# Kernel optimization log

Measured on AMD Instinct MI355X. Metric: run time of the kernel, lower is better.

Reference implementation:

```python
import jax, jax.numpy as jnp
import numpy as np

N_LINKS = 10000
N_PATHS = 50000
PLEN = 5                 # fixed path length -> max_len
E = N_PATHS * PLEN       # number of (link, path) edge entries
D = 32                   # link_state_dim == path_state_dim
H = 32
RU = 256                 # readout_units
T_ITERS = 8              # message-passing iterations t


def setup_inputs() -> dict:
    key = jax.random.key(0)
    ks = jax.random.split(key, 20)
    s = 0.1
    inp = {}
    inp["traffic"] = jax.random.uniform(ks[0], (N_PATHS,), dtype=jnp.float32)
    inp["packets"] = jax.random.uniform(ks[1], (N_PATHS,), dtype=jnp.float32)
    inp["time_dist_params"] = jax.random.normal(ks[2], (N_PATHS, 12), dtype=jnp.float32)
    inp["capacity"] = jax.random.uniform(ks[3], (N_LINKS,), dtype=jnp.float32)
    # edge lists: each path has exactly PLEN links
    inp["link_to_path"] = jax.random.randint(ks[4], (E,), 0, N_LINKS, dtype=jnp.int32)
    inp["path_ids"] = jnp.repeat(jnp.arange(N_PATHS, dtype=jnp.int32), PLEN)
    inp["sequence_path"] = jnp.tile(jnp.arange(PLEN, dtype=jnp.int32), N_PATHS)
    inp["path_to_link"] = jax.random.randint(ks[5], (E,), 0, N_PATHS, dtype=jnp.int32)
    inp["sequence_links"] = jax.random.randint(ks[6], (E,), 0, N_LINKS, dtype=jnp.int32)
    inp["n_links"] = N_LINKS
    inp["n_paths"] = N_PATHS
    # path-update GRU (input D -> hidden H), torch layout [3H, in]
    inp["Wi_p"] = jax.random.normal(ks[7], (3 * H, D), dtype=jnp.float32) * s
    inp["Wh_p"] = jax.random.normal(ks[8], (3 * H, H), dtype=jnp.float32) * s
    inp["bi_p"] = jnp.zeros((3 * H,), jnp.float32)
    inp["bh_p"] = jnp.zeros((3 * H,), jnp.float32)
    # link-update GRUCell (input H -> hidden D)
    inp["Wi_l"] = jax.random.normal(ks[9], (3 * D, H), dtype=jnp.float32) * s
    inp["Wh_l"] = jax.random.normal(ks[10], (3 * D, D), dtype=jnp.float32) * s
    inp["bi_l"] = jnp.zeros((3 * D,), jnp.float32)
    inp["bh_l"] = jnp.zeros((3 * D,), jnp.float32)
    # readout MLP
    inp["W1"] = jax.random.normal(ks[11], (RU, H), dtype=jnp.float32) * s
    inp["b1"] = jnp.zeros((RU,), jnp.float32)
    inp["W2"] = jax.random.normal(ks[12], (RU, RU), dtype=jnp.float32) * s
    inp["b2"] = jnp.zeros((RU,), jnp.float32)
    inp["W3"] = jax.random.normal(ks[13], (1, RU), dtype=jnp.float32) * s
    inp["b3"] = jnp.zeros((1,), jnp.float32)
    return inp


def _gru_step(x, h, Wi, Wh, bi, bh):
    # torch GRU gate math
    gi = x @ Wi.T + bi
    gh = h @ Wh.T + bh
    ir, iz, in_ = jnp.split(gi, 3, axis=-1)
    hr, hz, hn = jnp.split(gh, 3, axis=-1)
    r = jax.nn.sigmoid(ir + hr)
    z = jax.nn.sigmoid(iz + hz)
    n = jnp.tanh(in_ + r * hn)
    return (1.0 - z) * n + z * h


def reference(traffic, packets, time_dist_params, capacity,
              link_to_path, path_ids, sequence_path, path_to_link, sequence_links,
              n_links, n_paths,
              Wi_p, Wh_p, bi_p, bh_p, Wi_l, Wh_l, bi_l, bh_l,
              W1, b1, W2, b2, W3, b3):
    max_len = PLEN  # == sequence_path.max() + 1 (static)
    # per-path valid lengths (equivalent to the torch nonzero-row count loop)
    lens = jax.ops.segment_max(sequence_path, path_ids, num_segments=n_paths) + 1
    link_state = jnp.concatenate(
        [capacity[:, None], jnp.zeros((n_links, D - 1), capacity.dtype)], axis=1)
    path_state = jnp.concatenate(
        [traffic[:, None], packets[:, None], time_dist_params,
         jnp.zeros((n_paths, D - 14), traffic.dtype)], axis=1)

    for _ in range(T_ITERS):
        link_gather = link_state[link_to_path]  # [E, D]
        link_inputs = jnp.zeros((n_paths, max_len, D), link_state.dtype)
        link_inputs = link_inputs.at[path_ids, sequence_path].set(link_gather)

        def step(h, xt_t):
            xt, t = xt_t
            h_new = _gru_step(xt, h, Wi_p, Wh_p, bi_p, bh_p)
            h = jnp.where((t < lens)[:, None], h_new, h)  # pack_padded semantics
            return h, None

        path_state, _ = jax.lax.scan(
            step, path_state,
            (jnp.swapaxes(link_inputs, 0, 1), jnp.arange(max_len)))

        path_gather = path_state[path_to_link]  # [E, H]
        path_sum = jnp.zeros((n_links, H), path_gather.dtype).at[sequence_links].add(path_gather)
        link_state = _gru_step(path_sum, link_state, Wi_l, Wh_l, bi_l, bh_l)

    r = jax.nn.relu(path_state @ W1.T + b1)
    r = jax.nn.relu(r @ W2.T + b2)
    r = r @ W3.T + b3            # [n_paths, 1]
    return r[:, 0][None, :]      # [1, n_paths]
```

## Files before the change

### kernel.cpp

```cpp
#include <hip/hip_runtime.h>

#define NP 50000
#define NL 10000
#define PLEN 5
#define NE (NP * PLEN)
#define DD 32
#define RUU 256
#define TITERS 8
#define PPB 16
#define LPB 16
#define RPB 32

__device__ __forceinline__ float sigmoidf_(float a) {
    return 1.0f / (1.0f + __expf(-a));
}
__device__ __forceinline__ float tanhf_(float a) {
    a = fminf(fmaxf(a, -15.0f), 15.0f);
    float t = __expf(2.0f * a);
    return (t - 1.0f) / (t + 1.0f);
}

__global__ __launch_bounds__(256) void k_init(
    const float* __restrict__ traffic, const float* __restrict__ packets,
    const float* __restrict__ tdp, const float* __restrict__ capacity,
    float* __restrict__ path_state, float* __restrict__ link_state,
    int* __restrict__ lens, int* __restrict__ cnt) {
    int i = blockIdx.x * 256 + threadIdx.x;
    if (i < NP) {
        float v[DD];
        v[0] = traffic[i];
        v[1] = packets[i];
#pragma unroll
        for (int k = 0; k < 12; k++) v[2 + k] = tdp[i * 12 + k];
#pragma unroll
        for (int k = 14; k < DD; k++) v[k] = 0.0f;
#pragma unroll
        for (int k = 0; k < DD; k++) path_state[i * DD + k] = v[k];
        lens[i] = 0;
    }
    if (i < NL) {
        link_state[i * DD] = capacity[i];
#pragma unroll
        for (int k = 1; k < DD; k++) link_state[i * DD + k] = 0.0f;
        cnt[i] = 0;
    }
}

__global__ __launch_bounds__(256) void k_lens(const int* __restrict__ path_ids,
                                              const int* __restrict__ seq_path,
                                              int* __restrict__ lens) {
    int e = blockIdx.x * 256 + threadIdx.x;
    if (e < NE) atomicMax(&lens[path_ids[e]], seq_path[e] + 1);
}

__global__ __launch_bounds__(256) void k_csr_count(const int* __restrict__ seq_links,
                                                   int* __restrict__ cnt) {
    int e = blockIdx.x * 256 + threadIdx.x;
    if (e < NE) atomicAdd(&cnt[seq_links[e]], 1);
}

__global__ __launch_bounds__(256) void k_csr_scan(const int* __restrict__ cnt,
                                                  int* __restrict__ offs,
                                                  int* __restrict__ cursor) {
    __shared__ int ssum[256];
    const int tid = threadIdx.x;
    const int CH = 40;
    int base = tid * CH;
    int s = 0;
    for (int i = 0; i < CH; i++) {
        int idx = base + i;
        s += (idx < NL) ? cnt[idx] : 0;
    }
    ssum[tid] = s;
    __syncthreads();
    for (int off = 1; off < 256; off <<= 1) {
        int t = (tid >= off) ? ssum[tid - off] : 0;
        __syncthreads();
        ssum[tid] += t;
        __syncthreads();
    }
    int run = ssum[tid] - s;
    for (int i = 0; i < CH; i++) {
        int idx = base + i;
        if (idx < NL) {
            offs[idx] = run;
            cursor[idx] = run;
            run += cnt[idx];
        }
    }
    if (tid == 0) offs[NL] = ssum[255];
}

__global__ __launch_bounds__(256) void k_csr_fill(const int* __restrict__ seq_links,
                                                  const int* __restrict__ path_to_link,
                                                  int* __restrict__ cursor,
                                                  int* __restrict__ csr_pids) {
    int e = blockIdx.x * 256 + threadIdx.x;
    if (e < NE) {
        int l = seq_links[e];
        int slot = atomicAdd(&cursor[l], 1);
        csr_pids[slot] = path_to_link[e];
    }
}

__global__ __launch_bounds__(256) void k_w2t(const float* __restrict__ W2,
                                             float* __restrict__ W2t) {
    int j = blockIdx.x, k = threadIdx.x;
    W2t[k * RUU + j] = W2[j * RUU + k];
}

__global__ __launch_bounds__(256, 4) void k_gru_paths(
    const float* __restrict__ link_state, float* __restrict__ path_state,
    const int* __restrict__ link_to_path, const int* __restrict__ lens,
    const float* __restrict__ Wi, const float* __restrict__ Wh,
    const float* __restrict__ bi, const float* __restrict__ bh) {
    __shared__ float gi[PPB * PLEN * 96];
    __shared__ float hbuf[4][DD];
    const int tid = threadIdx.x;
    const int wave = tid >> 6;
    const int lane = tid & 63;
    const int d = lane & 31;
    const int half = lane >> 5;
    const int pl0 = wave * 4;
    const int pbase = blockIdx.x * PPB;

    float w[3][16];
#pragma unroll
    for (int g = 0; g < 3; g++) {
        const float* wp = &Wi[(g * 32 + d) * 32 + half * 16];
#pragma unroll
        for (int c = 0; c < 4; c++) *(float4*)&w[g][c * 4] = *(const float4*)&wp[c * 4];
    }
#pragma unroll
    for (int g = 0; g < 3; g++)
#pragma unroll
        for (int k = 0; k < 16; k++) asm volatile("" : "+v"(w[g][k]));
    {
        const float b0 = bi[d], b1_ = bi[d + 32], b2_ = bi[d + 64];
        for (int j = 0; j < 4; j++) {
            const int p = pbase + pl0 + j;
#pragma unroll
            for (int st = 0; st < PLEN; st++) {
                const int li = link_to_path[p * PLEN + st];
                float xk[16];
#pragma unroll
                for (int c = 0; c < 4; c++)
                    *(float4*)&xk[c * 4] =
                        *(const float4*)&link_state[li * DD + half * 16 + c * 4];
                float s0 = 0.f, s1 = 0.f, s2 = 0.f;
#pragma unroll
                for (int k = 0; k < 16; k++) {
                    s0 = fmaf(xk[k], w[0][k], s0);
                    s1 = fmaf(xk[k], w[1][k], s1);
                    s2 = fmaf(xk[k], w[2][k], s2);
                }
                s0 += __shfl_xor(s0, 32);
                s1 += __shfl_xor(s1, 32);
                s2 += __shfl_xor(s2, 32);
                float* gp = &gi[((pl0 + j) * PLEN + st) * 96];
                gp[d]      = s0 + b0;
                gp[d + 32] = s1 + b1_;
                gp[d + 64] = s2 + b2_;
            }
        }
    }
    __syncthreads();

#pragma unroll
    for (int g = 0; g < 3; g++) {
        const float* wp = &Wh[(g * 32 + d) * 32 + half * 16];
#pragma unroll
        for (int c = 0; c < 4; c++) *(float4*)&w[g][c * 4] = *(const float4*)&wp[c * 4];
    }
#pragma unroll
    for (int g = 0; g < 3; g++)
#pragma unroll
        for (int k = 0; k < 16; k++) asm volatile("" : "+v"(w[g][k]));
    const float bh0 = bh[d], bh1 = bh[d + 32], bh2 = bh[d + 64];

    for (int j = 0; j < 4; j++) {
        const int p = pbase + pl0 + j;
        const int len = lens[p];
        float hd = path_state[p * DD + d];
        float hk[16];
#pragma unroll
        for (int c = 0; c < 4; c++)
            *(float4*)&hk[c * 4] = *(const float4*)&path_state[p * DD + half * 16 + c * 4];
#pragma unroll
        for (int st = 0; st < PLEN; st++) {
            float hr = 0.f, hz = 0.f, hn = 0.f;
#pragma unroll
            for (int k = 0; k < 16; k++) {
                hr = fmaf(hk[k], w[0][k], hr);
                hz = fmaf(hk[k], w[1][k], hz);
                hn = fmaf(hk[k], w[2][k], hn);
            }
            hr += __shfl_xor(hr, 32);
            hz += __shfl_xor(hz, 32);
            hn += __shfl_xor(hn, 32);
            const float* gp = &gi[((pl0 + j) * PLEN + st) * 96];
            float gir = gp[d], giz = gp[d + 32], gin = gp[d + 64];
            float r = sigmoidf_(gir + hr + bh0);
            float z = sigmoidf_(giz + hz + bh1);
            float n = tanhf_(gin + r * (hn + bh2));
            float hnew = (1.0f - z) * n + z * hd;
            hd = (st < len) ? hnew : hd;
            hbuf[wave][d] = hd;
#pragma unroll
            for (int c = 0; c < 4; c++)
                *(float4*)&hk[c * 4] = *(const float4*)&hbuf[wave][half * 16 + c * 4];
        }
        if (half == 0) path_state[p * DD + d] = hd;
    }
}

__global__ __launch_bounds__(256, 4) void k_links(
    const float* __restrict__ path_state, float* __restrict__ link_state,
    const int* __restrict__ offs, const int* __restrict__ csr_pids,
    const float* __restrict__ Wi, const float* __restrict__ Wh,
    const float* __restrict__ bi, const float* __restrict__ bh) {
    __shared__ float xsum[4][4][DD];
    __shared__ float gil[4][4][96];
    const int tid = threadIdx.x;
    const int wave = tid >> 6;
    const int lane = tid & 63;
    const int d = lane & 31;
    const int half = lane >> 5;
    const int lbase = blockIdx.x * LPB + wave * 4;

    for (int j = 0; j < 4; j++) {
        const int l = lbase + j;
        const int beg = offs[l], end = offs[l + 1];
        float xv = 0.f;
        int t = beg + half;
        int pid = (t < end) ? csr_pids[t] : 0;
        while (t < end) {
            int t2 = t + 2;
            int pid2 = (t2 < end) ? csr_pids[t2] : 0;
            xv += path_state[pid * DD + d];
            pid = pid2;
            t = t2;
        }
        xv += __shfl_xor(xv, 32);
        xsum[wave][j][d] = xv;
    }
    __syncthreads();

    float w[3][16];
#pragma unroll
    for (int g = 0; g < 3; g++) {
        const float* wp = &Wi[(g * 32 + d) * 32 + half * 16];
#pragma unroll
        for (int c = 0; c < 4; c++) *(float4*)&w[g][c * 4] = *(const float4*)&wp[c * 4];
    }
#pragma unroll
    for (int g = 0; g < 3; g++)
#pragma unroll
        for (int k = 0; k < 16; k++) asm volatile("" : "+v"(w[g][k]));
    {
        const float b0 = bi[d], b1_ = bi[d + 32], b2_ = bi[d + 64];
        for (int j = 0; j < 4; j++) {
            float xk[16];
#pragma unroll
            for (int c = 0; c < 4; c++)
                *(float4*)&xk[c * 4] = *(const float4*)&xsum[wave][j][half * 16 + c * 4];
            float s0 = 0.f, s1 = 0.f, s2 = 0.f;
#pragma unroll
            for (int k = 0; k < 16; k++) {
                s0 = fmaf(xk[k], w[0][k], s0);
                s1 = fmaf(xk[k], w[1][k], s1);
                s2 = fmaf(xk[k], w[2][k], s2);
            }
            s0 += __shfl_xor(s0, 32);
            s1 += __shfl_xor(s1, 32);
            s2 += __shfl_xor(s2, 32);
            gil[wave][j][d]      = s0 + b0;
            gil[wave][j][d + 32] = s1 + b1_;
            gil[wave][j][d + 64] = s2 + b2_;
        }
    }
    __syncthreads();

#pragma unroll
    for (int g = 0; g < 3; g++) {
        const float* wp = &Wh[(g * 32 + d) * 32 + half * 16];
#pragma unroll
        for (int c = 0; c < 4; c++) *(float4*)&w[g][c * 4] = *(const float4*)&wp[c * 4];
    }
#pragma unroll
    for (int g = 0; g < 3; g++)
#pragma unroll
        for (int k = 0; k < 16; k++) asm volatile("" : "+v"(w[g][k]));
    const float bh0 = bh[d], bh1 = bh[d + 32], bh2 = bh[d + 64];
    for (int j = 0; j < 4; j++) {
        const int l = lbase + j;
        float hd = link_state[l * DD + d];
        float hk[16];
#pragma unroll
        for (int c = 0; c < 4; c++)
            *(float4*)&hk[c * 4] = *(const float4*)&link_state[l * DD + half * 16 + c * 4];
        float hr = 0.f, hz = 0.f, hn = 0.f;
#pragma unroll
        for (int k = 0; k < 16; k++) {
            hr = fmaf(hk[k], w[0][k], hr);
            hz = fmaf(hk[k], w[1][k], hz);
            hn = fmaf(hk[k], w[2][k], hn);
        }
        hr += __shfl_xor(hr, 32);
        hz += __shfl_xor(hz, 32);
        hn += __shfl_xor(hn, 32);
        float gir = gil[wave][j][d], giz = gil[wave][j][d + 32], gin = gil[wave][j][d + 64];
        float r = sigmoidf_(gir + hr + bh0);
        float z = sigmoidf_(giz + hz + bh1);
        float n = tanhf_(gin + r * (hn + bh2));
        float hnew = (1.0f - z) * n + z * hd;
        if (half == 0) link_state[l * DD + d] = hnew;
    }
}

__global__ __launch_bounds__(256, 4) void k_readout(
    const float* __restrict__ path_state, float* __restrict__ out,
    const float* __restrict__ W1, const float* __restrict__ b1,
    const float* __restrict__ W2t, const float* __restrict__ b2,
    const float* __restrict__ W3, const float* __restrict__ b3) {
    __shared__ float sr1[RPB * RUU];
    const int tid = threadIdx.x;
    const int p0 = blockIdx.x * RPB;

    float w1r[DD];
#pragma unroll
    for (int c = 0; c < 8; c++)
        *(float4*)&w1r[c * 4] = *(const float4*)&W1[tid * DD + c * 4];
    float bb1 = b1[tid];

#pragma unroll 2
    for (int m = 0; m < RPB; m++) {
        int p = p0 + m;
        if (p >= NP) p = NP - 1;
        const float4* xr = (const float4*)&path_state[(size_t)p * DD];
        float acc = bb1;
#pragma unroll
        for (int c = 0; c < 8; c++) {
            float4 xv = xr[c];
            acc = fmaf(xv.x, w1r[c * 4 + 0], fmaf(xv.y, w1r[c * 4 + 1],
                  fmaf(xv.z, w1r[c * 4 + 2], fmaf(xv.w, w1r[c * 4 + 3], acc))));
        }
        sr1[m * RUU + tid] = fmaxf(acc, 0.0f);
    }
    __syncthreads();

    const int pig = tid >> 5;
    const int jg  = tid & 31;
    float accs[4][8];
#pragma unroll
    for (int jj = 0; jj < 8; jj++) {
        float bv = b2[jg * 8 + jj];
#pragma unroll
        for (int pp = 0; pp < 4; pp++) accs[pp][jj] = bv;
    }
    for (int k4 = 0; k4 < 64; k4++) {
        const int k0 = k4 * 4;
        float a[4][4];
#pragma unroll
        for (int pp = 0; pp < 4; pp++)
            *(float4*)&a[pp][0] = *(const float4*)&sr1[(pig * 4 + pp) * RUU + k0];
#pragma unroll
        for (int kk = 0; kk < 4; kk++) {
            float4 w0 = *(const float4*)&W2t[(size_t)(k0 + kk) * RUU + jg * 8];
            float4 w1_ = *(const float4*)&W2t[(size_t)(k0 + kk) * RUU + jg * 8 + 4];
#pragma unroll
            for (int pp = 0; pp < 4; pp++) {
                float av = a[pp][kk];
                accs[pp][0] = fmaf(av, w0.x, accs[pp][0]);
                accs[pp][1] = fmaf(av, w0.y, accs[pp][1]);
                accs[pp][2] = fmaf(av, w0.z, accs[pp][2]);
                accs[pp][3] = fmaf(av, w0.w, accs[pp][3]);
                accs[pp][4] = fmaf(av, w1_.x, accs[pp][4]);
                accs[pp][5] = fmaf(av, w1_.y, accs[pp][5]);
                accs[pp][6] = fmaf(av, w1_.z, accs[pp][6]);
                accs[pp][7] = fmaf(av, w1_.w, accs[pp][7]);
            }
        }
    }

    float w3r[8];
#pragma unroll
    for (int c = 0; c < 2; c++)
        *(float4*)&w3r[c * 4] = *(const float4*)&W3[jg * 8 + c * 4];
    float val[4];
#pragma unroll
    for (int pp = 0; pp < 4; pp++) {
        float v = 0.f;
#pragma unroll
        for (int jj = 0; jj < 8; jj++) v = fmaf(w3r[jj], fmaxf(accs[pp][jj], 0.f), v);
        val[pp] = v;
    }
#pragma unroll
    for (int m = 1; m < 32; m <<= 1)
#pragma unroll
        for (int pp = 0; pp < 4; pp++) val[pp] += __shfl_xor(val[pp], m);
    if (jg == 0) {
        float b3v = b3[0];
#pragma unroll
        for (int pp = 0; pp < 4; pp++) {
            int p = p0 + pig * 4 + pp;
            if (p < NP) out[p] = val[pp] + b3v;
        }
    }
}

extern "C" void kernel_launch(void* const* d_in, const int* in_sizes, int n_in,
                              void* d_out, int out_size, void* d_ws, size_t ws_size,
                              hipStream_t stream) {
    const float* traffic  = (const float*)d_in[0];
    const float* packets  = (const float*)d_in[1];
    const float* tdp      = (const float*)d_in[2];
    const float* capacity = (const float*)d_in[3];
    const int* link_to_path = (const int*)d_in[4];
    const int* path_ids     = (const int*)d_in[5];
    const int* seq_path     = (const int*)d_in[6];
    const int* path_to_link = (const int*)d_in[7];
    const int* seq_links    = (const int*)d_in[8];
    const float* Wi_p = (const float*)d_in[11];
    const float* Wh_p = (const float*)d_in[12];
    const float* bi_p = (const float*)d_in[13];
    const float* bh_p = (const float*)d_in[14];
    const float* Wi_l = (const float*)d_in[15];
    const float* Wh_l = (const float*)d_in[16];
    const float* bi_l = (const float*)d_in[17];
    const float* bh_l = (const float*)d_in[18];
    const float* W1 = (const float*)d_in[19];
    const float* b1 = (const float*)d_in[20];
    const float* W2 = (const float*)d_in[21];
    const float* b2 = (const float*)d_in[22];
    const float* W3 = (const float*)d_in[23];
    const float* b3 = (const float*)d_in[24];
    float* out = (float*)d_out;

    float* path_state = (float*)d_ws;
    float* link_state = path_state + (size_t)NP * DD;
    float* w2t        = link_state + (size_t)NL * DD;
    int* lens     = (int*)(w2t + RUU * RUU);
    int* cnt      = lens + NP;
    int* offs     = cnt + NL;
    int* cursor   = offs + NL + 1;
    int* csr_pids = cursor + NL;

    k_init<<<(NP + 255) / 256, 256, 0, stream>>>(traffic, packets, tdp, capacity,
                                                 path_state, link_state, lens, cnt);
    k_lens<<<(NE + 255) / 256, 256, 0, stream>>>(path_ids, seq_path, lens);
    k_csr_count<<<(NE + 255) / 256, 256, 0, stream>>>(seq_links, cnt);
    k_csr_scan<<<1, 256, 0, stream>>>(cnt, offs, cursor);
    k_csr_fill<<<(NE + 255) / 256, 256, 0, stream>>>(seq_links, path_to_link,
                                                     cursor, csr_pids);
    k_w2t<<<RUU, RUU, 0, stream>>>(W2, w2t);
    for (int t = 0; t < TITERS; t++) {
        k_gru_paths<<<NP / PPB, 256, 0, stream>>>(
            link_state, path_state, link_to_path, lens, Wi_p, Wh_p, bi_p, bh_p);
        k_links<<<NL / LPB, 256, 0, stream>>>(
            path_state, link_state, offs, csr_pids, Wi_l, Wh_l, bi_l, bh_l);
    }
    k_readout<<<(NP + RPB - 1) / RPB, 256, 0, stream>>>(path_state, out, W1, b1,
                                                        w2t, b2, W3, b3);
}
```

Before: 1.364 ms.

## Assign one link per wave and software-pipeline path-kernel link gathers

The link kernel now handles one link per wave (LPB 4) instead of four, so there are four times as many blocks. Its CSR gather loop is unrolled with four independent accumulators to keep more loads in flight. In the path kernel, all link indices are loaded first and the 20 link-state gathers are software-pipelined so the next row is fetched while the current one is used in FMAs. The goal is more memory-level parallelism and better latency hiding, at the cost of reloading weights more often per link and higher register pressure.

After: 1.304 ms. 1.05x faster.

```diff
diff --git a/kernel.cpp b/kernel.cpp
--- a/kernel.cpp
+++ b/kernel.cpp
@@ -8,7 +8,7 @@
 #define RUU 256
 #define TITERS 8
 #define PPB 16
-#define LPB 16
+#define LPB 4
 #define RPB 32
 
 __device__ __forceinline__ float sigmoidf_(float a) {
@@ -137,30 +137,44 @@
         for (int k = 0; k < 16; k++) asm volatile("" : "+v"(w[g][k]));
     {
         const float b0 = bi[d], b1_ = bi[d + 32], b2_ = bi[d + 64];
+        int lia[4 * PLEN];
+#pragma unroll
         for (int j = 0; j < 4; j++) {
             const int p = pbase + pl0 + j;
 #pragma unroll
-            for (int st = 0; st < PLEN; st++) {
-                const int li = link_to_path[p * PLEN + st];
-                float xk[16];
+            for (int s = 0; s < PLEN; s++) lia[j * PLEN + s] = link_to_path[p * PLEN + s];
+        }
+        float xk[16];
+#pragma unroll
+        for (int c = 0; c < 4; c++)
+            *(float4*)&xk[c * 4] =
+                *(const float4*)&link_state[lia[0] * DD + half * 16 + c * 4];
+#pragma unroll
+        for (int u = 0; u < 20; u++) {
+            float xn[16];
+            if (u + 1 < 20) {
 #pragma unroll
                 for (int c = 0; c < 4; c++)
-                    *(float4*)&xk[c * 4] =
-                        *(const float4*)&link_state[li * DD + half * 16 + c * 4];
-                float s0 = 0.f, s1 = 0.f, s2 = 0.f;
-#pragma unroll
-                for (int k = 0; k < 16; k++) {
-                    s0 = fmaf(xk[k], w[0][k], s0);
-                    s1 = fmaf(xk[k], w[1][k], s1);
-                    s2 = fmaf(xk[k], w[2][k], s2);
-                }
-                s0 += __shfl_xor(s0, 32);
-                s1 += __shfl_xor(s1, 32);
-                s2 += __shfl_xor(s2, 32);
-                float* gp = &gi[((pl0 + j) * PLEN + st) * 96];
-                gp[d]      = s0 + b0;
-                gp[d + 32] = s1 + b1_;
-                gp[d + 64] = s2 + b2_;
+                    *(float4*)&xn[c * 4] =
+                        *(const float4*)&link_state[lia[u + 1] * DD + half * 16 + c * 4];
+            }
+            float s0 = 0.f, s1 = 0.f, s2 = 0.f;
+#pragma unroll
+            for (int k = 0; k < 16; k++) {
+                s0 = fmaf(xk[k], w[0][k], s0);
+                s1 = fmaf(xk[k], w[1][k], s1);
+                s2 = fmaf(xk[k], w[2][k], s2);
+            }
+            s0 += __shfl_xor(s0, 32);
+            s1 += __shfl_xor(s1, 32);
+            s2 += __shfl_xor(s2, 32);
+            float* gp = &gi[(pl0 + (u / 5)) * (PLEN * 96) + (u % 5) * 96];
+            gp[d]      = s0 + b0;
+            gp[d + 32] = s1 + b1_;
+            gp[d + 64] = s2 + b2_;
+            if (u + 1 < 20) {
+#pragma unroll
+                for (int k = 0; k < 16; k++) xk[k] = xn[k];
             }
         }
     }
@@ -219,32 +233,14 @@
     const int* __restrict__ offs, const int* __restrict__ csr_pids,
     const float* __restrict__ Wi, const float* __restrict__ Wh,
     const float* __restrict__ bi, const float* __restrict__ bh) {
-    __shared__ float xsum[4][4][DD];
-    __shared__ float gil[4][4][96];
+    __shared__ float xsum[4][DD];
+    __shared__ float gil[4][96];
     const int tid = threadIdx.x;
     const int wave = tid >> 6;
     const int lane = tid & 63;
     const int d = lane & 31;
     const int half = lane >> 5;
-    const int lbase = blockIdx.x * LPB + wave * 4;
-
-    for (int j = 0; j < 4; j++) {
-        const int l = lbase + j;
-        const int beg = offs[l], end = offs[l + 1];
-        float xv = 0.f;
-        int t = beg + half;
-        int pid = (t < end) ? csr_pids[t] : 0;
-        while (t < end) {
-            int t2 = t + 2;
-            int pid2 = (t2 < end) ? csr_pids[t2] : 0;
-            xv += path_state[pid * DD + d];
-            pid = pid2;
-            t = t2;
-        }
-        xv += __shfl_xor(xv, 32);
-        xsum[wave][j][d] = xv;
-    }
-    __syncthreads();
+    const int l = blockIdx.x * LPB + wave;
 
     float w[3][16];
 #pragma unroll
@@ -257,27 +253,45 @@
     for (int g = 0; g < 3; g++)
 #pragma unroll
         for (int k = 0; k < 16; k++) asm volatile("" : "+v"(w[g][k]));
+
+    const int beg = offs[l], end = offs[l + 1];
+    float a0 = 0.f, a1 = 0.f, a2 = 0.f, a3 = 0.f;
+    int t = beg + half;
+    for (; t + 6 < end; t += 8) {
+        int q0 = csr_pids[t];
+        int q1 = csr_pids[t + 2];
+        int q2 = csr_pids[t + 4];
+        int q3 = csr_pids[t + 6];
+        a0 += path_state[q0 * DD + d];
+        a1 += path_state[q1 * DD + d];
+        a2 += path_state[q2 * DD + d];
+        a3 += path_state[q3 * DD + d];
+    }
+    for (; t < end; t += 2) a0 += path_state[csr_pids[t] * DD + d];
+    float xv = (a0 + a1) + (a2 + a3);
+    xv += __shfl_xor(xv, 32);
+    xsum[wave][d] = xv;
+    __syncthreads();
+
     {
         const float b0 = bi[d], b1_ = bi[d + 32], b2_ = bi[d + 64];
-        for (int j = 0; j < 4; j++) {
-            float xk[16];
-#pragma unroll
-            for (int c = 0; c < 4; c++)
-                *(float4*)&xk[c * 4] = *(const float4*)&xsum[wave][j][half * 16 + c * 4];
-            float s0 = 0.f, s1 = 0.f, s2 = 0.f;
-#pragma unroll
-            for (int k = 0; k < 16; k++) {
-                s0 = fmaf(xk[k], w[0][k], s0);
-                s1 = fmaf(xk[k], w[1][k], s1);
-                s2 = fmaf(xk[k], w[2][k], s2);
-            }
-            s0 += __shfl_xor(s0, 32);
-            s1 += __shfl_xor(s1, 32);
-            s2 += __shfl_xor(s2, 32);
-            gil[wave][j][d]      = s0 + b0;
-            gil[wave][j][d + 32] = s1 + b1_;
-            gil[wave][j][d + 64] = s2 + b2_;
-        }
+        float xk[16];
+#pragma unroll
+        for (int c = 0; c < 4; c++)
+            *(float4*)&xk[c * 4] = *(const float4*)&xsum[wave][half * 16 + c * 4];
+        float s0 = 0.f, s1 = 0.f, s2 = 0.f;
+#pragma unroll
+        for (int k = 0; k < 16; k++) {
+            s0 = fmaf(xk[k], w[0][k], s0);
+            s1 = fmaf(xk[k], w[1][k], s1);
+            s2 = fmaf(xk[k], w[2][k], s2);
+        }
+        s0 += __shfl_xor(s0, 32);
+        s1 += __shfl_xor(s1, 32);
+        s2 += __shfl_xor(s2, 32);
+        gil[wave][d]      = s0 + b0;
+        gil[wave][d + 32] = s1 + b1_;
+        gil[wave][d + 64] = s2 + b2_;
     }
     __syncthreads();
 
@@ -292,8 +306,7 @@
 #pragma unroll
         for (int k = 0; k < 16; k++) asm volatile("" : "+v"(w[g][k]));
     const float bh0 = bh[d], bh1 = bh[d + 32], bh2 = bh[d + 64];
-    for (int j = 0; j < 4; j++) {
-        const int l = lbase + j;
+    {
         float hd = link_state[l * DD + d];
         float hk[16];
 #pragma unroll
@@ -309,7 +322,7 @@
         hr += __shfl_xor(hr, 32);
         hz += __shfl_xor(hz, 32);
         hn += __shfl_xor(hn, 32);
-        float gir = gil[wave][j][d], giz = gil[wave][j][d + 32], gin = gil[wave][j][d + 64];
+        float gir = gil[wave][d], giz = gil[wave][d + 32], gin = gil[wave][d + 64];
         float r = sigmoidf_(gir + hr + bh0);
         float z = sigmoidf_(giz + hz + bh1);
         float n = tanhf_(gin + r * (hn + bh2));
```

## Fuse path-to-link scatter into path GRU via float atomics, prefetch link gathers

Applied to the files above, without the earlier changes.

Replaces the link-side CSR gather of path states with a path-side CSR that lets each path GRU block atomically add its final hidden state into a per-link sum buffer, which the link kernel reads and then zeroes. This removes a second pass over path_state in the link kernel and its irregular gather. It adds 250k×32 float atomics per iteration, which contend on about 10k links and make the summation order nondeterministic. The input-projection loop in the path kernel is also flattened and software-pipelined so the next link_state row is loaded while the current one is being processed.

Result: no change. 1.376 ms (+0.8%).

```diff
diff --git a/kernel.cpp b/kernel.cpp
--- a/kernel.cpp
+++ b/kernel.cpp
@@ -24,7 +24,8 @@
     const float* __restrict__ traffic, const float* __restrict__ packets,
     const float* __restrict__ tdp, const float* __restrict__ capacity,
     float* __restrict__ path_state, float* __restrict__ link_state,
-    int* __restrict__ lens, int* __restrict__ cnt) {
+    float* __restrict__ path_sum, int* __restrict__ lens,
+    int* __restrict__ cnt_p) {
     int i = blockIdx.x * 256 + threadIdx.x;
     if (i < NP) {
         float v[DD];
@@ -37,12 +38,14 @@
 #pragma unroll
         for (int k = 0; k < DD; k++) path_state[i * DD + k] = v[k];
         lens[i] = 0;
+        cnt_p[i] = 0;
     }
     if (i < NL) {
         link_state[i * DD] = capacity[i];
 #pragma unroll
         for (int k = 1; k < DD; k++) link_state[i * DD + k] = 0.0f;
-        cnt[i] = 0;
+#pragma unroll
+        for (int k = 0; k < DD; k++) path_sum[i * DD + k] = 0.0f;
     }
 }
 
@@ -53,23 +56,23 @@
     if (e < NE) atomicMax(&lens[path_ids[e]], seq_path[e] + 1);
 }
 
-__global__ __launch_bounds__(256) void k_csr_count(const int* __restrict__ seq_links,
-                                                   int* __restrict__ cnt) {
+__global__ __launch_bounds__(256) void k_csr_count_p(
+    const int* __restrict__ path_to_link, int* __restrict__ cnt_p) {
     int e = blockIdx.x * 256 + threadIdx.x;
-    if (e < NE) atomicAdd(&cnt[seq_links[e]], 1);
-}
-
-__global__ __launch_bounds__(256) void k_csr_scan(const int* __restrict__ cnt,
-                                                  int* __restrict__ offs,
-                                                  int* __restrict__ cursor) {
+    if (e < NE) atomicAdd(&cnt_p[path_to_link[e]], 1);
+}
+
+__global__ __launch_bounds__(256) void k_csr_scan_p(const int* __restrict__ cnt_p,
+                                                    int* __restrict__ offs_p,
+                                                    int* __restrict__ cursor_p) {
     __shared__ int ssum[256];
     const int tid = threadIdx.x;
-    const int CH = 40;
+    const int CH = 196;
     int base = tid * CH;
     int s = 0;
     for (int i = 0; i < CH; i++) {
         int idx = base + i;
-        s += (idx < NL) ? cnt[idx] : 0;
+        s += (idx < NP) ? cnt_p[idx] : 0;
     }
     ssum[tid] = s;
     __syncthreads();
@@ -82,24 +85,23 @@
     int run = ssum[tid] - s;
     for (int i = 0; i < CH; i++) {
         int idx = base + i;
-        if (idx < NL) {
-            offs[idx] = run;
-            cursor[idx] = run;
-            run += cnt[idx];
-        }
-    }
-    if (tid == 0) offs[NL] = ssum[255];
-}
-
-__global__ __launch_bounds__(256) void k_csr_fill(const int* __restrict__ seq_links,
-                                                  const int* __restrict__ path_to_link,
-                                                  int* __restrict__ cursor,
-                                                  int* __restrict__ csr_pids) {
+        if (idx < NP) {
+            offs_p[idx] = run;
+            cursor_p[idx] = run;
+            run += cnt_p[idx];
+        }
+    }
+    if (tid == 0) offs_p[NP] = ssum[255];
+}
+
+__global__ __launch_bounds__(256) void k_csr_fill_p(
+    const int* __restrict__ path_to_link, const int* __restrict__ seq_links,
+    int* __restrict__ cursor_p, int* __restrict__ csr_lids) {
     int e = blockIdx.x * 256 + threadIdx.x;
     if (e < NE) {
-        int l = seq_links[e];
-        int slot = atomicAdd(&cursor[l], 1);
-        csr_pids[slot] = path_to_link[e];
+        int p = path_to_link[e];
+        int slot = atomicAdd(&cursor_p[p], 1);
+        csr_lids[slot] = seq_links[e];
     }
 }
 
@@ -112,6 +114,8 @@
 __global__ __launch_bounds__(256, 4) void k_gru_paths(
     const float* __restrict__ link_state, float* __restrict__ path_state,
     const int* __restrict__ link_to_path, const int* __restrict__ lens,
+    const int* __restrict__ offs_p, const int* __restrict__ csr_lids,
+    float* __restrict__ path_sum,
     const float* __restrict__ Wi, const float* __restrict__ Wh,
     const float* __restrict__ bi, const float* __restrict__ bh) {
     __shared__ float gi[PPB * PLEN * 96];
@@ -137,30 +141,44 @@
         for (int k = 0; k < 16; k++) asm volatile("" : "+v"(w[g][k]));
     {
         const float b0 = bi[d], b1_ = bi[d + 32], b2_ = bi[d + 64];
+        int lia[4 * PLEN];
+#pragma unroll
         for (int j = 0; j < 4; j++) {
             const int p = pbase + pl0 + j;
 #pragma unroll
-            for (int st = 0; st < PLEN; st++) {
-                const int li = link_to_path[p * PLEN + st];
-                float xk[16];
+            for (int s = 0; s < PLEN; s++) lia[j * PLEN + s] = link_to_path[p * PLEN + s];
+        }
+        float xk[16];
+#pragma unroll
+        for (int c = 0; c < 4; c++)
+            *(float4*)&xk[c * 4] =
+                *(const float4*)&link_state[lia[0] * DD + half * 16 + c * 4];
+#pragma unroll
+        for (int u = 0; u < 20; u++) {
+            float xn[16];
+            if (u + 1 < 20) {
 #pragma unroll
                 for (int c = 0; c < 4; c++)
-                    *(float4*)&xk[c * 4] =
-                        *(const float4*)&link_state[li * DD + half * 16 + c * 4];
-                float s0 = 0.f, s1 = 0.f, s2 = 0.f;
-#pragma unroll
-                for (int k = 0; k < 16; k++) {
-                    s0 = fmaf(xk[k], w[0][k], s0);
-                    s1 = fmaf(xk[k], w[1][k], s1);
-                    s2 = fmaf(xk[k], w[2][k], s2);
-                }
-                s0 += __shfl_xor(s0, 32);
-                s1 += __shfl_xor(s1, 32);
-                s2 += __shfl_xor(s2, 32);
-                float* gp = &gi[((pl0 + j) * PLEN + st) * 96];
-                gp[d]      = s0 + b0;
-                gp[d + 32] = s1 + b1_;
-                gp[d + 64] = s2 + b2_;
+                    *(float4*)&xn[c * 4] =
+                        *(const float4*)&link_state[lia[u + 1] * DD + half * 16 + c * 4];
+            }
+            float s0 = 0.f, s1 = 0.f, s2 = 0.f;
+#pragma unroll
+            for (int k = 0; k < 16; k++) {
+                s0 = fmaf(xk[k], w[0][k], s0);
+                s1 = fmaf(xk[k], w[1][k], s1);
+                s2 = fmaf(xk[k], w[2][k], s2);
+            }
+            s0 += __shfl_xor(s0, 32);
+            s1 += __shfl_xor(s1, 32);
+            s2 += __shfl_xor(s2, 32);
+            float* gp = &gi[(pl0 + (u / 5)) * (PLEN * 96) + (u % 5) * 96];
+            gp[d]      = s0 + b0;
+            gp[d + 32] = s1 + b1_;
+            gp[d + 64] = s2 + b2_;
+            if (u + 1 < 20) {
+#pragma unroll
+                for (int k = 0; k < 16; k++) xk[k] = xn[k];
             }
         }
     }
@@ -211,15 +229,18 @@
                 *(float4*)&hk[c * 4] = *(const float4*)&hbuf[wave][half * 16 + c * 4];
         }
         if (half == 0) path_state[p * DD + d] = hd;
+        const int eb = offs_p[p], ee = offs_p[p + 1];
+        for (int e = eb + half; e < ee; e += 2) {
+            const int l = csr_lids[e];
+            atomicAdd(&path_sum[l * DD + d], hd);
+        }
     }
 }
 
 __global__ __launch_bounds__(256, 4) void k_links(
-    const float* __restrict__ path_state, float* __restrict__ link_state,
-    const int* __restrict__ offs, const int* __restrict__ csr_pids,
+    float* __restrict__ path_sum, float* __restrict__ link_state,
     const float* __restrict__ Wi, const float* __restrict__ Wh,
     const float* __restrict__ bi, const float* __restrict__ bh) {
-    __shared__ float xsum[4][4][DD];
     __shared__ float gil[4][4][96];
     const int tid = threadIdx.x;
     const int wave = tid >> 6;
@@ -228,24 +249,6 @@
     const int half = lane >> 5;
     const int lbase = blockIdx.x * LPB + wave * 4;
 
-    for (int j = 0; j < 4; j++) {
-        const int l = lbase + j;
-        const int beg = offs[l], end = offs[l + 1];
-        float xv = 0.f;
-        int t = beg + half;
-        int pid = (t < end) ? csr_pids[t] : 0;
-        while (t < end) {
-            int t2 = t + 2;
-            int pid2 = (t2 < end) ? csr_pids[t2] : 0;
-            xv += path_state[pid * DD + d];
-            pid = pid2;
-            t = t2;
-        }
-        xv += __shfl_xor(xv, 32);
-        xsum[wave][j][d] = xv;
-    }
-    __syncthreads();
-
     float w[3][16];
 #pragma unroll
     for (int g = 0; g < 3; g++) {
@@ -260,10 +263,11 @@
     {
         const float b0 = bi[d], b1_ = bi[d + 32], b2_ = bi[d + 64];
         for (int j = 0; j < 4; j++) {
+            const int l = lbase + j;
             float xk[16];
 #pragma unroll
             for (int c = 0; c < 4; c++)
-                *(float4*)&xk[c * 4] = *(const float4*)&xsum[wave][j][half * 16 + c * 4];
+                *(float4*)&xk[c * 4] = *(const float4*)&path_sum[l * DD + half * 16 + c * 4];
             float s0 = 0.f, s1 = 0.f, s2 = 0.f;
 #pragma unroll
             for (int k = 0; k < 16; k++) {
@@ -277,6 +281,7 @@
             gil[wave][j][d]      = s0 + b0;
             gil[wave][j][d + 32] = s1 + b1_;
             gil[wave][j][d + 64] = s2 + b2_;
+            path_sum[l * DD + d] = 0.0f;
         }
     }
     __syncthreads();
@@ -439,26 +444,29 @@
 
     float* path_state = (float*)d_ws;
     float* link_state = path_state + (size_t)NP * DD;
-    float* w2t        = link_state + (size_t)NL * DD;
+    float* path_sum   = link_state + (size_t)NL * DD;
+    float* w2t        = path_sum + (size_t)NL * DD;
     int* lens     = (int*)(w2t + RUU * RUU);
-    int* cnt      = lens + NP;
-    int* offs     = cnt + NL;
-    int* cursor   = offs + NL + 1;
-    int* csr_pids = cursor + NL;
+    int* cnt_p    = lens + NP;
+    int* offs_p   = cnt_p + NP;
+    int* cursor_p = offs_p + NP + 1;
+    int* csr_lids = cursor_p + NP;
 
     k_init<<<(NP + 255) / 256, 256, 0, stream>>>(traffic, packets, tdp, capacity,
-                                                 path_state, link_state, lens, cnt);
+                                                 path_state, link_state, path_sum,
+                                                 lens, cnt_p);
     k_lens<<<(NE + 255) / 256, 256, 0, stream>>>(path_ids, seq_path, lens);
-    k_csr_count<<<(NE + 255) / 256, 256, 0, stream>>>(seq_links, cnt);
-    k_csr_scan<<<1, 256, 0, stream>>>(cnt, offs, cursor);
-    k_csr_fill<<<(NE + 255) / 256, 256, 0, stream>>>(seq_links, path_to_link,
-                                                     cursor, csr_pids);
+    k_csr_count_p<<<(NE + 255) / 256, 256, 0, stream>>>(path_to_link, cnt_p);
+    k_csr_scan_p<<<1, 256, 0, stream>>>(cnt_p, offs_p, cursor_p);
+    k_csr_fill_p<<<(NE + 255) / 256, 256, 0, stream>>>(path_to_link, seq_links,
+                                                       cursor_p, csr_lids);
     k_w2t<<<RUU, RUU, 0, stream>>>(W2, w2t);
     for (int t = 0; t < TITERS; t++) {
         k_gru_paths<<<NP / PPB, 256, 0, stream>>>(
-            link_state, path_state, link_to_path, lens, Wi_p, Wh_p, bi_p, bh_p);
+            link_state, path_state, link_to_path, lens, offs_p, csr_lids,
+            path_sum, Wi_p, Wh_p, bi_p, bh_p);
         k_links<<<NL / LPB, 256, 0, stream>>>(
-            path_state, link_state, offs, csr_pids, Wi_l, Wh_l, bi_l, bh_l);
+            path_sum, link_state, Wi_l, Wh_l, bi_l, bh_l);
     }
     k_readout<<<(NP + RPB - 1) / RPB, 256, 0, stream>>>(path_state, out, W1, b1,
                                                         w2t, b2, W3, b3);
```
